# Optimization experiments

Hardware: AMD Instinct MI355X
Metric: run time of the kernel (lower is better)

## Reference

```python
import jax, jax.numpy as jnp
import numpy as np

N_NODES = 50000
N_EDGES = 800000
IN_CH, HID_CH, OUT_CH = 128, 256, 128


def _glorot(key, shape):
    fan_in, fan_out = shape[1], shape[0]
    lim = float(np.sqrt(6.0 / (fan_in + fan_out)))
    return jax.random.uniform(key, shape, jnp.float32, -lim, lim)


def setup_inputs() -> dict:
    key = jax.random.key(0)
    ks = jax.random.split(key, 8)
    x = jax.random.normal(ks[0], (N_NODES, IN_CH), jnp.float32)
    edge_index = jax.random.randint(ks[1], (2, N_EDGES), 0, N_NODES, jnp.int64)
    return {
        "x": x,
        "edge_index": edge_index,
        # layer 1: SAGEConv(128 -> 256): lin_l (with bias) on aggregated, lin_r (no bias) on root
        "W1l": _glorot(ks[2], (HID_CH, IN_CH)),
        "b1l": jnp.zeros((HID_CH,), jnp.float32),
        "W1r": _glorot(ks[3], (HID_CH, IN_CH)),
        # layer 2: SAGEConv(256 -> 128)
        "W2l": _glorot(ks[4], (OUT_CH, HID_CH)),
        "b2l": jnp.zeros((OUT_CH,), jnp.float32),
        "W2r": _glorot(ks[5], (OUT_CH, HID_CH)),
    }


def _sage_conv(x, src, dst, Wl, bl, Wr, n_nodes):
    # mean-aggregate neighbor (source) features at destination nodes
    msg = x[src]                                                   # [E, C] gather
    agg = jax.ops.segment_sum(msg, dst, num_segments=n_nodes)      # [N, C]
    deg = jax.ops.segment_sum(jnp.ones((src.shape[0],), x.dtype), dst,
                              num_segments=n_nodes)                # [N]
    mean = agg / jnp.maximum(deg, 1.0)[:, None]                    # zero-degree -> 0
    return mean @ Wl.T + bl + x @ Wr.T


def reference(x, edge_index, W1l, b1l, W1r, W2l, b2l, W2r):
    src, dst = edge_index[0], edge_index[1]
    n = x.shape[0]
    h = _sage_conv(x, src, dst, W1l, b1l, W1r, n)
    h = jax.nn.relu(h)  # dropout is identity in eval mode
    out = _sage_conv(h, src, dst, W2l, b2l, W2r, n)
    return out
```

## Files before the change

kernel.cpp:

```cpp
#include <hip/hip_runtime.h>

#define N_NODES 50000
#define IN_CH   128
#define HID_CH  256
#define OUT_CH  128

#define NB    196
#define NWG   64
#define NBNW  (NB * NWG)
#define SCHUNK 49

#define XBLK  3125
#define WBLK  64

typedef __attribute__((ext_vector_type(8))) short bf16x8;
typedef __attribute__((ext_vector_type(4))) float f32x4;
typedef __attribute__((ext_vector_type(2))) float f32x2;

__device__ __forceinline__ unsigned short f32_bf16_rne(float f) {
    unsigned u = __float_as_uint(f);
    unsigned r = u + 0x7fff + ((u >> 16) & 1);
    return (unsigned short)(r >> 16);
}

__device__ __forceinline__ void cvt8(const float* __restrict__ in,
                                     unsigned short* __restrict__ outp, size_t j)
{
    const float4* p = reinterpret_cast<const float4*>(in) + 2 * j;
    float4 a = p[0], b = p[1];
    alignas(16) unsigned short t[8] = {
        f32_bf16_rne(a.x), f32_bf16_rne(a.y), f32_bf16_rne(a.z), f32_bf16_rne(a.w),
        f32_bf16_rne(b.x), f32_bf16_rne(b.y), f32_bf16_rne(b.z), f32_bf16_rne(b.w)};
    *reinterpret_cast<int4*>(outp + 8 * j) = *reinterpret_cast<const int4*>(t);
}

__global__ __launch_bounds__(256) void prep_kernel(
    const int* __restrict__ src, const int* __restrict__ dst,
    int* __restrict__ counts, int E, int chunk,
    const float* __restrict__ x, unsigned short* __restrict__ xb,
    unsigned char* __restrict__ xb8,
    const float* __restrict__ W1l, const float* __restrict__ W1r,
    const float* __restrict__ W2l, const float* __restrict__ W2r,
    unsigned short* __restrict__ W1lb, unsigned short* __restrict__ W1rb,
    unsigned short* __restrict__ W2lb, unsigned short* __restrict__ W2rb)
{
    const int b = blockIdx.x;
    if (b < NWG) {
        __shared__ int h[NB];
        for (int i = threadIdx.x; i < NB; i += 256) h[i] = 0;
        __syncthreads();
        const int e0 = b * chunk;
        const int e1 = min(e0 + chunk, E);
        for (int e = e0 + threadIdx.x; e < e1; e += 256) {
            int s = src[e], d = dst[e];
            if ((unsigned)s < (unsigned)N_NODES && (unsigned)d < (unsigned)N_NODES)
                atomicAdd(&h[d >> 8], 1);
        }
        __syncthreads();
        for (int i = threadIdx.x; i < NB; i += 256)
            counts[i * NWG + b] = h[i];
    } else if (b < NWG + XBLK) {
        size_t j = (size_t)(b - NWG) * 256 + threadIdx.x;
        const float4* p = reinterpret_cast<const float4*>(x) + 2 * j;
        float4 a = p[0], bb = p[1];
        alignas(16) unsigned short t[8] = {
            f32_bf16_rne(a.x),  f32_bf16_rne(a.y),  f32_bf16_rne(a.z),  f32_bf16_rne(a.w),
            f32_bf16_rne(bb.x), f32_bf16_rne(bb.y), f32_bf16_rne(bb.z), f32_bf16_rne(bb.w)};
        *reinterpret_cast<int4*>(xb + 8 * j) = *reinterpret_cast<const int4*>(t);
        unsigned u0 = __builtin_amdgcn_cvt_pk_fp8_f32(a.x, a.y, 0, false);
        u0 = __builtin_amdgcn_cvt_pk_fp8_f32(a.z, a.w, u0, true);
        unsigned u1 = __builtin_amdgcn_cvt_pk_fp8_f32(bb.x, bb.y, 0, false);
        u1 = __builtin_amdgcn_cvt_pk_fp8_f32(bb.z, bb.w, u1, true);
        uint2 uv; uv.x = u0; uv.y = u1;
        *reinterpret_cast<uint2*>(xb8 + 8 * j) = uv;
    } else {
        int idx = (b - NWG - XBLK) * 256 + threadIdx.x;
        int seg = idx >> 12, j = idx & 4095;
        const float* in = (seg == 0) ? W1l : (seg == 1) ? W1r : (seg == 2) ? W2l : W2r;
        unsigned short* o = (seg == 0) ? W1lb : (seg == 1) ? W1rb : (seg == 2) ? W2lb : W2rb;
        cvt8(in, o, (size_t)j);
    }
}

__global__ __launch_bounds__(256) void scan_all_kernel(
    const int* __restrict__ counts, int* __restrict__ S)
{
    __shared__ int tot[256];
    const int t = threadIdx.x;
    const int base = t * SCHUNK;
    int loc[SCHUNK];
    int sum = 0;
#pragma unroll
    for (int k = 0; k < SCHUNK; ++k) {
        loc[k] = sum;
        sum += counts[base + k];
    }
    tot[t] = sum;
    __syncthreads();
    for (int off = 1; off < 256; off <<= 1) {
        int v = (t >= off) ? tot[t - off] : 0;
        __syncthreads();
        if (t >= off) tot[t] += v;
        __syncthreads();
    }
    int offv = (t == 0) ? 0 : tot[t - 1];
#pragma unroll
    for (int k = 0; k < SCHUNK; ++k)
        S[base + k] = loc[k] + offv;
    if (t == 255) S[NBNW] = offv + sum;
}

__global__ __launch_bounds__(256) void bscatter_kernel(
    const int* __restrict__ src, const int* __restrict__ dst,
    const int* __restrict__ S, int* __restrict__ pairs, int E, int chunk)
{
    __shared__ int cur[NB];
    const int w = blockIdx.x;
    for (int i = threadIdx.x; i < NB; i += 256) cur[i] = S[i * NWG + w];
    __syncthreads();
    const int e0 = w * chunk;
    const int e1 = min(e0 + chunk, E);
    for (int e = e0 + threadIdx.x; e < e1; e += 256) {
        int s = src[e], d = dst[e];
        if ((unsigned)s < (unsigned)N_NODES && (unsigned)d < (unsigned)N_NODES) {
            int pos = atomicAdd(&cur[d >> 8], 1);
            pairs[pos] = (s << 8) | (d & 255);
        }
    }
}

__global__ __launch_bounds__(256) void bsort_kernel(
    const int* __restrict__ pairs, const int* __restrict__ S,
    int* __restrict__ rowptr, int* __restrict__ colidx)
{
    __shared__ int hcnt[256];
    __shared__ int hcur[256];
    const int b = blockIdx.x;
    const int start = S[b * NWG];
    const int endv  = (b == NB - 1) ? S[NBNW] : S[(b + 1) * NWG];

    hcnt[threadIdx.x] = 0;
    __syncthreads();
    for (int e = start + threadIdx.x; e < endv; e += 256)
        atomicAdd(&hcnt[pairs[e] & 255], 1);
    __syncthreads();
    for (int off = 1; off < 256; off <<= 1) {
        int t = (threadIdx.x >= off) ? hcnt[threadIdx.x - off] : 0;
        __syncthreads();
        if (threadIdx.x >= off) hcnt[threadIdx.x] += t;
        __syncthreads();
    }
    int offv = (threadIdx.x == 0) ? 0 : hcnt[threadIdx.x - 1];
    hcur[threadIdx.x] = offv;
    int node = (b << 8) + threadIdx.x;
    if (node < N_NODES) rowptr[node] = start + offv;
    if (b == NB - 1 && threadIdx.x == 0) rowptr[N_NODES] = endv;
    __syncthreads();
    for (int e = start + threadIdx.x; e < endv; e += 256) {
        int p = pairs[e];
        int pos = atomicAdd(&hcur[p & 255], 1);
        colidx[start + pos] = (unsigned)p >> 8;
    }
}

#define ACC8(v)                                                              \
    { f32x2 t0 = __builtin_amdgcn_cvt_pk_f32_fp8(v.x, false);                \
      f32x2 t1 = __builtin_amdgcn_cvt_pk_f32_fp8(v.x, true);                 \
      f32x2 t2 = __builtin_amdgcn_cvt_pk_f32_fp8(v.y, false);                \
      f32x2 t3 = __builtin_amdgcn_cvt_pk_f32_fp8(v.y, true);                 \
      acc[0] += t0.x; acc[1] += t0.y; acc[2] += t1.x; acc[3] += t1.y;        \
      acc[4] += t2.x; acc[5] += t2.y; acc[6] += t3.x; acc[7] += t3.y; }

#define AGG_BODY(CH)                                                            \
    const int node = blockIdx.x * 4 + (threadIdx.x >> 6);                       \
    if (node >= N_NODES) return;                                                \
    const int lane = threadIdx.x & 63;                                          \
    const int grp = lane >> 4, ch = lane & 15;                                  \
    const int beg = rowptr[node], end = rowptr[node + 1];                       \
    const int len = end - beg;                                                  \
    const int q = (len + 3) >> 2;                                               \
    int j  = beg + grp * q;                                                     \
    int j1 = min(j + q, end);                                                   \
    float acc[8] = {};                                                          \
    for (; j + 3 < j1; j += 4) {                                                \
        int s0 = colidx[j],     s1 = colidx[j + 1];                             \
        int s2 = colidx[j + 2], s3 = colidx[j + 3];                             \
        uint2 v0 = *reinterpret_cast<const uint2*>(feat + (size_t)s0 * CH + ch * 8); \
        uint2 v1 = *reinterpret_cast<const uint2*>(feat + (size_t)s1 * CH + ch * 8); \
        uint2 v2 = *reinterpret_cast<const uint2*>(feat + (size_t)s2 * CH + ch * 8); \
        uint2 v3 = *reinterpret_cast<const uint2*>(feat + (size_t)s3 * CH + ch * 8); \
        ACC8(v0) ACC8(v1) ACC8(v2) ACC8(v3)                                     \
    }                                                                           \
    for (; j < j1; ++j) {                                                       \
        int s0 = colidx[j];                                                     \
        uint2 v0 = *reinterpret_cast<const uint2*>(feat + (size_t)s0 * CH + ch * 8); \
        ACC8(v0)                                                                \
    }                                                                           \
    _Pragma("unroll")                                                           \
    for (int k = 0; k < 8; ++k) {                                               \
        acc[k] += __shfl_xor(acc[k], 16);                                       \
        acc[k] += __shfl_xor(acc[k], 32);                                       \
    }                                                                           \
    const float sc = 1.0f / fmaxf((float)len, 1.0f);

__global__ __launch_bounds__(256) void agg1_kernel(
    const unsigned char* __restrict__ feat, const int* __restrict__ rowptr,
    const int* __restrict__ colidx, unsigned short* __restrict__ outp)
{
    AGG_BODY(IN_CH)
    if (grp == 0) {
        alignas(16) unsigned short t[8];
#pragma unroll
        for (int k = 0; k < 8; ++k) t[k] = f32_bf16_rne(acc[k] * sc);
        *reinterpret_cast<int4*>(outp + (size_t)node * IN_CH + ch * 8) =
            *reinterpret_cast<const int4*>(t);
    }
}

__global__ __launch_bounds__(256) void agg2_kernel(
    const unsigned char* __restrict__ feat, const int* __restrict__ rowptr,
    const int* __restrict__ colidx, float* __restrict__ out)
{
    AGG_BODY(OUT_CH)
    if (grp == 0) {
        float* o = out + (size_t)node * OUT_CH + ch * 8;
        float4 o0 = reinterpret_cast<float4*>(o)[0];
        float4 o1 = reinterpret_cast<float4*>(o)[1];
        o0.x += acc[0] * sc; o0.y += acc[1] * sc; o0.z += acc[2] * sc; o0.w += acc[3] * sc;
        o1.x += acc[4] * sc; o1.y += acc[5] * sc; o1.z += acc[6] * sc; o1.w += acc[7] * sc;
        reinterpret_cast<float4*>(o)[0] = o0;
        reinterpret_cast<float4*>(o)[1] = o1;
    }
}

__device__ __forceinline__ void stage_async(
    const unsigned short* __restrict__ g, int ldg, int rowBase, int maxRow,
    int kBase, unsigned short* __restrict__ s, int tid)
{
    const int wave = tid >> 6;
    const int lane = tid & 63;
    const int r_in = lane >> 3;
    const int c_g  = (lane & 7) ^ r_in;
#pragma unroll
    for (int it = 0; it < 4; ++it) {
        const int rowBlk = it * 32 + wave * 8;
        int row = rowBase + rowBlk + r_in;
        if (row >= maxRow) row = maxRow - 1;
        const unsigned short* gp = g + (size_t)row * ldg + kBase + c_g * 8;
        unsigned short* lp = s + rowBlk * 64;
        __builtin_amdgcn_global_load_lds(
            (const __attribute__((address_space(1))) unsigned int*)gp,
            (__attribute__((address_space(3))) unsigned int*)lp,
            16, 0, 0);
    }
}

__device__ __forceinline__ const bf16x8* frag_ptr(
    const unsigned short* __restrict__ s, int rr, int c)
{
    return reinterpret_cast<const bf16x8*>(s + rr * 64 + (((c ^ (rr & 7))) << 3));
}

__device__ __forceinline__ void mfma_tile(
    const unsigned short* __restrict__ As, const unsigned short* __restrict__ Bs,
    int wm, int wn, int l16, int quad, f32x4 acc[4][4])
{
#pragma unroll
    for (int k0 = 0; k0 < 64; k0 += 32) {
        const int c = (k0 >> 3) + quad;
        bf16x8 a[4], b[4];
#pragma unroll
        for (int i = 0; i < 4; ++i)
            a[i] = *frag_ptr(As, wm * 64 + i * 16 + l16, c);
#pragma unroll
        for (int j = 0; j < 4; ++j)
            b[j] = *frag_ptr(Bs, wn * 64 + j * 16 + l16, c);
#pragma unroll
        for (int i = 0; i < 4; ++i)
#pragma unroll
            for (int j = 0; j < 4; ++j)
                acc[i][j] = __builtin_amdgcn_mfma_f32_16x16x32_bf16(
                    b[j], a[i], acc[i][j], 0, 0, 0);
    }
}

__global__ __launch_bounds__(256) void gemm1_mfma(
    const unsigned short* __restrict__ mean1b, const unsigned short* __restrict__ xb,
    const unsigned short* __restrict__ W1lb,   const unsigned short* __restrict__ W1rb,
    const float* __restrict__ b1l, unsigned short* __restrict__ hb)
{
    __shared__ unsigned short As[128 * 64];
    __shared__ unsigned short Bs[128 * 64];
    const int tid = threadIdx.x;
    const int wid = tid >> 6, lane = tid & 63;
    const int wm = wid & 1, wn = wid >> 1;
    const int l16 = lane & 15, quad = lane >> 4;
    const int rowBase = blockIdx.x * 128;
    const int colBase = blockIdx.y * 128;

    f32x4 z = {0.f, 0.f, 0.f, 0.f};
    f32x4 acc[4][4];
#pragma unroll
    for (int i = 0; i < 4; ++i)
#pragma unroll
        for (int j = 0; j < 4; ++j) acc[i][j] = z;

#pragma unroll
    for (int op = 0; op < 2; ++op) {
        const unsigned short* A = op ? xb : mean1b;
        const unsigned short* B = op ? W1rb : W1lb;
#pragma unroll
        for (int kb = 0; kb < IN_CH; kb += 64) {
            __syncthreads();
            stage_async(A, IN_CH, rowBase, N_NODES, kb, As, tid);
            stage_async(B, IN_CH, colBase, HID_CH, kb, Bs, tid);
            __syncthreads();
            mfma_tile(As, Bs, wm, wn, l16, quad, acc);
        }
    }

#pragma unroll
    for (int i = 0; i < 4; ++i) {
        int m = rowBase + wm * 64 + i * 16 + l16;
        if (m >= N_NODES) continue;
#pragma unroll
        for (int j = 0; j < 4; ++j) {
            int col = colBase + wn * 64 + j * 16 + quad * 4;
            float4 bv = *reinterpret_cast<const float4*>(b1l + col);
            alignas(8) unsigned short t[4];
            t[0] = f32_bf16_rne(fmaxf(acc[i][j][0] + bv.x, 0.0f));
            t[1] = f32_bf16_rne(fmaxf(acc[i][j][1] + bv.y, 0.0f));
            t[2] = f32_bf16_rne(fmaxf(acc[i][j][2] + bv.z, 0.0f));
            t[3] = f32_bf16_rne(fmaxf(acc[i][j][3] + bv.w, 0.0f));
            *reinterpret_cast<uint2*>(hb + (size_t)m * HID_CH + col) =
                *reinterpret_cast<const uint2*>(t);
        }
    }
}

__global__ __launch_bounds__(256) void gemm2_mfma(
    const unsigned short* __restrict__ hb, const unsigned short* __restrict__ W2lb,
    const unsigned short* __restrict__ W2rb, const float* __restrict__ b2l,
    unsigned char* __restrict__ pb8, float* __restrict__ out)
{
    __shared__ unsigned short As[128 * 64];
    __shared__ unsigned short Bs[128 * 64];
    const int tid = threadIdx.x;
    const int wid = tid >> 6, lane = tid & 63;
    const int wm = wid & 1, wn = wid >> 1;
    const int l16 = lane & 15, quad = lane >> 4;
    const int rowBase = blockIdx.x * 128;
    const unsigned short* B = blockIdx.y ? W2rb : W2lb;

    f32x4 z = {0.f, 0.f, 0.f, 0.f};
    f32x4 acc[4][4];
#pragma unroll
    for (int i = 0; i < 4; ++i)
#pragma unroll
        for (int j = 0; j < 4; ++j) acc[i][j] = z;

#pragma unroll
    for (int kb = 0; kb < HID_CH; kb += 64) {
        __syncthreads();
        stage_async(hb, HID_CH, rowBase, N_NODES, kb, As, tid);
        stage_async(B, HID_CH, 0, OUT_CH, kb, Bs, tid);
        __syncthreads();
        mfma_tile(As, Bs, wm, wn, l16, quad, acc);
    }

    if (blockIdx.y == 0) {
#pragma unroll
        for (int i = 0; i < 4; ++i) {
            int m = rowBase + wm * 64 + i * 16 + l16;
            if (m >= N_NODES) continue;
#pragma unroll
            for (int j = 0; j < 4; ++j) {
                int col = wn * 64 + j * 16 + quad * 4;
                unsigned u = __builtin_amdgcn_cvt_pk_fp8_f32(
                    acc[i][j][0], acc[i][j][1], 0, false);
                u = __builtin_amdgcn_cvt_pk_fp8_f32(
                    acc[i][j][2], acc[i][j][3], u, true);
                *reinterpret_cast<unsigned*>(pb8 + (size_t)m * OUT_CH + col) = u;
            }
        }
    } else {
#pragma unroll
        for (int i = 0; i < 4; ++i) {
            int m = rowBase + wm * 64 + i * 16 + l16;
            if (m >= N_NODES) continue;
#pragma unroll
            for (int j = 0; j < 4; ++j) {
                int col = wn * 64 + j * 16 + quad * 4;
                float4 bv = *reinterpret_cast<const float4*>(b2l + col);
                float4 o;
                o.x = acc[i][j][0] + bv.x;
                o.y = acc[i][j][1] + bv.y;
                o.z = acc[i][j][2] + bv.z;
                o.w = acc[i][j][3] + bv.w;
                *reinterpret_cast<float4*>(out + (size_t)m * OUT_CH + col) = o;
            }
        }
    }
}

extern "C" void kernel_launch(void* const* d_in, const int* in_sizes, int n_in,
                              void* d_out, int out_size, void* d_ws, size_t ws_size,
                              hipStream_t stream)
{
    const float* x   = (const float*)d_in[0];
    const int*   ei  = (const int*)d_in[1];
    const float* W1l = (const float*)d_in[2];
    const float* b1l = (const float*)d_in[3];
    const float* W1r = (const float*)d_in[4];
    const float* W2l = (const float*)d_in[5];
    const float* b2l = (const float*)d_in[6];
    const float* W2r = (const float*)d_in[7];

    const int E = in_sizes[1] / 2;
    const int* src = ei;
    const int* dst = ei + E;

    char* ws = (char*)d_ws;
    size_t off = 0;
    auto alloc = [&](size_t bytes) {
        void* p = ws + off;
        off += (bytes + 255) & ~(size_t)255;
        return p;
    };
    unsigned short* xb     = (unsigned short*)alloc((size_t)N_NODES * IN_CH * 2);
    unsigned char*  xb8    = (unsigned char*)alloc((size_t)N_NODES * IN_CH);
    unsigned short* mean1b = (unsigned short*)alloc((size_t)N_NODES * IN_CH * 2);
    unsigned short* hb     = (unsigned short*)alloc((size_t)N_NODES * HID_CH * 2);
    unsigned char*  pb8    = (unsigned char*)alloc((size_t)N_NODES * OUT_CH);
    unsigned short* W1lb   = (unsigned short*)alloc((size_t)HID_CH * IN_CH * 2);
    unsigned short* W1rb   = (unsigned short*)alloc((size_t)HID_CH * IN_CH * 2);
    unsigned short* W2lb   = (unsigned short*)alloc((size_t)OUT_CH * HID_CH * 2);
    unsigned short* W2rb   = (unsigned short*)alloc((size_t)OUT_CH * HID_CH * 2);
    int* counts = (int*)alloc((size_t)NBNW * 4);
    int* S      = (int*)alloc((size_t)(NBNW + 1) * 4);
    int* pairs  = (int*)alloc((size_t)E * 4);
    int* rowptr = (int*)alloc((size_t)(N_NODES + 1) * 4);
    int* colidx = (int*)alloc((size_t)E * 4);
    float* out = (float*)d_out;

    const int chunk = (E + NWG - 1) / NWG;

    prep_kernel<<<NWG + XBLK + WBLK, 256, 0, stream>>>(
        src, dst, counts, E, chunk, x, xb, xb8,
        W1l, W1r, W2l, W2r, W1lb, W1rb, W2lb, W2rb);
    scan_all_kernel<<<1, 256, 0, stream>>>(counts, S);
    bscatter_kernel<<<NWG, 256, 0, stream>>>(src, dst, S, pairs, E, chunk);
    bsort_kernel<<<NB, 256, 0, stream>>>(pairs, S, rowptr, colidx);

    const int aggBlocks = (N_NODES + 3) / 4;
    const int mBlocks = (N_NODES + 127) / 128;

    agg1_kernel<<<aggBlocks, 256, 0, stream>>>(xb8, rowptr, colidx, mean1b);
    gemm1_mfma<<<dim3(mBlocks, HID_CH / 128), 256, 0, stream>>>(
        mean1b, xb, W1lb, W1rb, b1l, hb);
    gemm2_mfma<<<dim3(mBlocks, 2), 256, 0, stream>>>(hb, W2lb, W2rb, b2l, pb8, out);
    agg2_kernel<<<aggBlocks, 256, 0, stream>>>(pb8, rowptr, colidx, out);
}
```

Measured before the change: 235.1 us.

## Replace two-level bucket sort CSR build with atomic counting sort; 16 lanes per node aggregation

The CSR construction drops the bucketed histogram, scan, scatter and per-bucket sort. It now uses global per-node atomic degree counts, a single-block scan over all 50000 nodes, and an atomic scatter of source ids into colidx. The neighbour aggregation now assigns 16 lanes per node instead of 64 split into four groups, and broadcasts column indices with sub-wave shuffles, which removes the cross-group reductions. This cuts kernel launches and a pass over a pairs buffer, but brings heavy global atomic contention, a serial single-block scan over many elements, and a non-deterministic neighbour order.

Result: slower. 399.0 us (+69.7%).

```diff
diff --git a/kernel.cpp b/kernel.cpp
--- a/kernel.cpp
+++ b/kernel.cpp
@@ -5,13 +5,10 @@
 #define HID_CH  256
 #define OUT_CH  128
 
-#define NB    196
 #define NWG   64
-#define NBNW  (NB * NWG)
-#define SCHUNK 49
-
 #define XBLK  3125
 #define WBLK  64
+#define SCHUNK 196
 
 typedef __attribute__((ext_vector_type(8))) short bf16x8;
 typedef __attribute__((ext_vector_type(4))) float f32x4;
@@ -46,19 +43,13 @@
 {
     const int b = blockIdx.x;
     if (b < NWG) {
-        __shared__ int h[NB];
-        for (int i = threadIdx.x; i < NB; i += 256) h[i] = 0;
-        __syncthreads();
         const int e0 = b * chunk;
         const int e1 = min(e0 + chunk, E);
         for (int e = e0 + threadIdx.x; e < e1; e += 256) {
             int s = src[e], d = dst[e];
             if ((unsigned)s < (unsigned)N_NODES && (unsigned)d < (unsigned)N_NODES)
-                atomicAdd(&h[d >> 8], 1);
-        }
-        __syncthreads();
-        for (int i = threadIdx.x; i < NB; i += 256)
-            counts[i * NWG + b] = h[i];
+                atomicAdd(&counts[d], 1);
+        }
     } else if (b < NWG + XBLK) {
         size_t j = (size_t)(b - NWG) * 256 + threadIdx.x;
         const float4* p = reinterpret_cast<const float4*>(x) + 2 * j;
@@ -82,18 +73,16 @@
     }
 }
 
-__global__ __launch_bounds__(256) void scan_all_kernel(
-    const int* __restrict__ counts, int* __restrict__ S)
+__global__ __launch_bounds__(256) void scan_kernel(
+    const int* __restrict__ counts, int* __restrict__ rowptr, int* __restrict__ cur)
 {
     __shared__ int tot[256];
     const int t = threadIdx.x;
     const int base = t * SCHUNK;
-    int loc[SCHUNK];
     int sum = 0;
-#pragma unroll
     for (int k = 0; k < SCHUNK; ++k) {
-        loc[k] = sum;
-        sum += counts[base + k];
+        int i = base + k;
+        if (i < N_NODES) sum += counts[i];
     }
     tot[t] = sum;
     __syncthreads();
@@ -103,63 +92,30 @@
         if (t >= off) tot[t] += v;
         __syncthreads();
     }
-    int offv = (t == 0) ? 0 : tot[t - 1];
-#pragma unroll
-    for (int k = 0; k < SCHUNK; ++k)
-        S[base + k] = loc[k] + offv;
-    if (t == 255) S[NBNW] = offv + sum;
-}
-
-__global__ __launch_bounds__(256) void bscatter_kernel(
+    int run = (t == 0) ? 0 : tot[t - 1];
+    for (int k = 0; k < SCHUNK; ++k) {
+        int i = base + k;
+        if (i < N_NODES) {
+            rowptr[i] = run;
+            cur[i]    = run;
+            run += counts[i];
+        }
+    }
+    if (t == 255) rowptr[N_NODES] = run;
+}
+
+__global__ __launch_bounds__(256) void scatter_kernel(
     const int* __restrict__ src, const int* __restrict__ dst,
-    const int* __restrict__ S, int* __restrict__ pairs, int E, int chunk)
-{
-    __shared__ int cur[NB];
-    const int w = blockIdx.x;
-    for (int i = threadIdx.x; i < NB; i += 256) cur[i] = S[i * NWG + w];
-    __syncthreads();
-    const int e0 = w * chunk;
-    const int e1 = min(e0 + chunk, E);
-    for (int e = e0 + threadIdx.x; e < e1; e += 256) {
+    int* __restrict__ cur, int* __restrict__ colidx, int E)
+{
+    int i = blockIdx.x * 256 + threadIdx.x;
+    const int stride = gridDim.x * 256;
+    for (int e = i; e < E; e += stride) {
         int s = src[e], d = dst[e];
         if ((unsigned)s < (unsigned)N_NODES && (unsigned)d < (unsigned)N_NODES) {
-            int pos = atomicAdd(&cur[d >> 8], 1);
-            pairs[pos] = (s << 8) | (d & 255);
-        }
-    }
-}
-
-__global__ __launch_bounds__(256) void bsort_kernel(
-    const int* __restrict__ pairs, const int* __restrict__ S,
-    int* __restrict__ rowptr, int* __restrict__ colidx)
-{
-    __shared__ int hcnt[256];
-    __shared__ int hcur[256];
-    const int b = blockIdx.x;
-    const int start = S[b * NWG];
-    const int endv  = (b == NB - 1) ? S[NBNW] : S[(b + 1) * NWG];
-
-    hcnt[threadIdx.x] = 0;
-    __syncthreads();
-    for (int e = start + threadIdx.x; e < endv; e += 256)
-        atomicAdd(&hcnt[pairs[e] & 255], 1);
-    __syncthreads();
-    for (int off = 1; off < 256; off <<= 1) {
-        int t = (threadIdx.x >= off) ? hcnt[threadIdx.x - off] : 0;
-        __syncthreads();
-        if (threadIdx.x >= off) hcnt[threadIdx.x] += t;
-        __syncthreads();
-    }
-    int offv = (threadIdx.x == 0) ? 0 : hcnt[threadIdx.x - 1];
-    hcur[threadIdx.x] = offv;
-    int node = (b << 8) + threadIdx.x;
-    if (node < N_NODES) rowptr[node] = start + offv;
-    if (b == NB - 1 && threadIdx.x == 0) rowptr[N_NODES] = endv;
-    __syncthreads();
-    for (int e = start + threadIdx.x; e < endv; e += 256) {
-        int p = pairs[e];
-        int pos = atomicAdd(&hcur[p & 255], 1);
-        colidx[start + pos] = (unsigned)p >> 8;
+            int pos = atomicAdd(&cur[d], 1);
+            colidx[pos] = s;
+        }
     }
 }
 
@@ -172,34 +128,30 @@
       acc[4] += t2.x; acc[5] += t2.y; acc[6] += t3.x; acc[7] += t3.y; }
 
 #define AGG_BODY(CH)                                                            \
-    const int node = blockIdx.x * 4 + (threadIdx.x >> 6);                       \
+    const int node = blockIdx.x * 16 + (threadIdx.x >> 4);                      \
     if (node >= N_NODES) return;                                                \
-    const int lane = threadIdx.x & 63;                                          \
-    const int grp = lane >> 4, ch = lane & 15;                                  \
+    const int l8 = threadIdx.x & 15;                                            \
     const int beg = rowptr[node], end = rowptr[node + 1];                       \
     const int len = end - beg;                                                  \
-    const int q = (len + 3) >> 2;                                               \
-    int j  = beg + grp * q;                                                     \
-    int j1 = min(j + q, end);                                                   \
     float acc[8] = {};                                                          \
-    for (; j + 3 < j1; j += 4) {                                                \
-        int s0 = colidx[j],     s1 = colidx[j + 1];                             \
-        int s2 = colidx[j + 2], s3 = colidx[j + 3];                             \
-        uint2 v0 = *reinterpret_cast<const uint2*>(feat + (size_t)s0 * CH + ch * 8); \
-        uint2 v1 = *reinterpret_cast<const uint2*>(feat + (size_t)s1 * CH + ch * 8); \
-        uint2 v2 = *reinterpret_cast<const uint2*>(feat + (size_t)s2 * CH + ch * 8); \
-        uint2 v3 = *reinterpret_cast<const uint2*>(feat + (size_t)s3 * CH + ch * 8); \
-        ACC8(v0) ACC8(v1) ACC8(v2) ACC8(v3)                                     \
-    }                                                                           \
-    for (; j < j1; ++j) {                                                       \
-        int s0 = colidx[j];                                                     \
-        uint2 v0 = *reinterpret_cast<const uint2*>(feat + (size_t)s0 * CH + ch * 8); \
-        ACC8(v0)                                                                \
-    }                                                                           \
-    _Pragma("unroll")                                                           \
-    for (int k = 0; k < 8; ++k) {                                               \
-        acc[k] += __shfl_xor(acc[k], 16);                                       \
-        acc[k] += __shfl_xor(acc[k], 32);                                       \
+    for (int base = beg; base < end; base += 16) {                              \
+        const int cnt = min(16, end - base);                                    \
+        int ci = colidx[base + ((l8 < cnt) ? l8 : 0)];                          \
+        int k = 0;                                                              \
+        for (; k + 3 < cnt; k += 4) {                                           \
+            int s0 = __shfl(ci, k, 16),     s1 = __shfl(ci, k + 1, 16);         \
+            int s2 = __shfl(ci, k + 2, 16), s3 = __shfl(ci, k + 3, 16);         \
+            uint2 v0 = *reinterpret_cast<const uint2*>(feat + (size_t)s0 * CH + l8 * 8); \
+            uint2 v1 = *reinterpret_cast<const uint2*>(feat + (size_t)s1 * CH + l8 * 8); \
+            uint2 v2 = *reinterpret_cast<const uint2*>(feat + (size_t)s2 * CH + l8 * 8); \
+            uint2 v3 = *reinterpret_cast<const uint2*>(feat + (size_t)s3 * CH + l8 * 8); \
+            ACC8(v0) ACC8(v1) ACC8(v2) ACC8(v3)                                 \
+        }                                                                       \
+        for (; k < cnt; ++k) {                                                  \
+            int s0 = __shfl(ci, k, 16);                                         \
+            uint2 v0 = *reinterpret_cast<const uint2*>(feat + (size_t)s0 * CH + l8 * 8); \
+            ACC8(v0)                                                            \
+        }                                                                       \
     }                                                                           \
     const float sc = 1.0f / fmaxf((float)len, 1.0f);
 
@@ -208,13 +160,11 @@
     const int* __restrict__ colidx, unsigned short* __restrict__ outp)
 {
     AGG_BODY(IN_CH)
-    if (grp == 0) {
-        alignas(16) unsigned short t[8];
-#pragma unroll
-        for (int k = 0; k < 8; ++k) t[k] = f32_bf16_rne(acc[k] * sc);
-        *reinterpret_cast<int4*>(outp + (size_t)node * IN_CH + ch * 8) =
-            *reinterpret_cast<const int4*>(t);
-    }
+    alignas(16) unsigned short t[8];
+#pragma unroll
+    for (int k = 0; k < 8; ++k) t[k] = f32_bf16_rne(acc[k] * sc);
+    *reinterpret_cast<int4*>(outp + (size_t)node * IN_CH + l8 * 8) =
+        *reinterpret_cast<const int4*>(t);
 }
 
 __global__ __launch_bounds__(256) void agg2_kernel(
@@ -222,15 +172,13 @@
     const int* __restrict__ colidx, float* __restrict__ out)
 {
     AGG_BODY(OUT_CH)
-    if (grp == 0) {
-        float* o = out + (size_t)node * OUT_CH + ch * 8;
-        float4 o0 = reinterpret_cast<float4*>(o)[0];
-        float4 o1 = reinterpret_cast<float4*>(o)[1];
-        o0.x += acc[0] * sc; o0.y += acc[1] * sc; o0.z += acc[2] * sc; o0.w += acc[3] * sc;
-        o1.x += acc[4] * sc; o1.y += acc[5] * sc; o1.z += acc[6] * sc; o1.w += acc[7] * sc;
-        reinterpret_cast<float4*>(o)[0] = o0;
-        reinterpret_cast<float4*>(o)[1] = o1;
-    }
+    float* o = out + (size_t)node * OUT_CH + l8 * 8;
+    float4 o0 = reinterpret_cast<float4*>(o)[0];
+    float4 o1 = reinterpret_cast<float4*>(o)[1];
+    o0.x += acc[0] * sc; o0.y += acc[1] * sc; o0.z += acc[2] * sc; o0.w += acc[3] * sc;
+    o1.x += acc[4] * sc; o1.y += acc[5] * sc; o1.z += acc[6] * sc; o1.w += acc[7] * sc;
+    reinterpret_cast<float4*>(o)[0] = o0;
+    reinterpret_cast<float4*>(o)[1] = o1;
 }
 
 __device__ __forceinline__ void stage_async(
@@ -436,23 +384,22 @@
     unsigned short* W1rb   = (unsigned short*)alloc((size_t)HID_CH * IN_CH * 2);
     unsigned short* W2lb   = (unsigned short*)alloc((size_t)OUT_CH * HID_CH * 2);
     unsigned short* W2rb   = (unsigned short*)alloc((size_t)OUT_CH * HID_CH * 2);
-    int* counts = (int*)alloc((size_t)NBNW * 4);
-    int* S      = (int*)alloc((size_t)(NBNW + 1) * 4);
-    int* pairs  = (int*)alloc((size_t)E * 4);
+    int* counts = (int*)alloc((size_t)N_NODES * 4);
     int* rowptr = (int*)alloc((size_t)(N_NODES + 1) * 4);
+    int* cur    = (int*)alloc((size_t)N_NODES * 4);
     int* colidx = (int*)alloc((size_t)E * 4);
     float* out = (float*)d_out;
 
     const int chunk = (E + NWG - 1) / NWG;
 
+    hipMemsetAsync(counts, 0, (size_t)N_NODES * 4, stream);
     prep_kernel<<<NWG + XBLK + WBLK, 256, 0, stream>>>(
         src, dst, counts, E, chunk, x, xb, xb8,
         W1l, W1r, W2l, W2r, W1lb, W1rb, W2lb, W2rb);
-    scan_all_kernel<<<1, 256, 0, stream>>>(counts, S);
-    bscatter_kernel<<<NWG, 256, 0, stream>>>(src, dst, S, pairs, E, chunk);
-    bsort_kernel<<<NB, 256, 0, stream>>>(pairs, S, rowptr, colidx);
-
-    const int aggBlocks = (N_NODES + 3) / 4;
+    scan_kernel<<<1, 256, 0, stream>>>(counts, rowptr, cur);
+    scatter_kernel<<<2048, 256, 0, stream>>>(src, dst, cur, colidx, E);
+
+    const int aggBlocks = (N_NODES + 15) / 16;
     const int mBlocks = (N_NODES + 127) / 128;
 
     agg1_kernel<<<aggBlocks, 256, 0, stream>>>(xb8, rowptr, colidx, mean1b);
```

## Map one 16-lane group per node in aggregation, broadcast neighbor indices via shuffles

Applied to the files above, without the earlier changes.

The aggregation kernels now assign 16 lanes per destination node, 16 nodes per block, instead of a 64-lane wave split into four edge partitions per node. This removes the cross-group shuffle reduction and the idle lanes during output. Each group loads up to 16 column indices cooperatively and broadcasts them with width-16 shuffles, replacing redundant per-lane index loads. In exchange, each node's edges are processed serially by one group, so per-node memory parallelism drops while more nodes run concurrently.

Result: faster. 219.6 us (-6.6%).

```diff
diff --git a/kernel.cpp b/kernel.cpp
--- a/kernel.cpp
+++ b/kernel.cpp
@@ -172,34 +172,30 @@
       acc[4] += t2.x; acc[5] += t2.y; acc[6] += t3.x; acc[7] += t3.y; }
 
 #define AGG_BODY(CH)                                                            \
-    const int node = blockIdx.x * 4 + (threadIdx.x >> 6);                       \
+    const int node = blockIdx.x * 16 + (threadIdx.x >> 4);                      \
     if (node >= N_NODES) return;                                                \
-    const int lane = threadIdx.x & 63;                                          \
-    const int grp = lane >> 4, ch = lane & 15;                                  \
+    const int l8 = threadIdx.x & 15;                                            \
     const int beg = rowptr[node], end = rowptr[node + 1];                       \
     const int len = end - beg;                                                  \
-    const int q = (len + 3) >> 2;                                               \
-    int j  = beg + grp * q;                                                     \
-    int j1 = min(j + q, end);                                                   \
     float acc[8] = {};                                                          \
-    for (; j + 3 < j1; j += 4) {                                                \
-        int s0 = colidx[j],     s1 = colidx[j + 1];                             \
-        int s2 = colidx[j + 2], s3 = colidx[j + 3];                             \
-        uint2 v0 = *reinterpret_cast<const uint2*>(feat + (size_t)s0 * CH + ch * 8); \
-        uint2 v1 = *reinterpret_cast<const uint2*>(feat + (size_t)s1 * CH + ch * 8); \
-        uint2 v2 = *reinterpret_cast<const uint2*>(feat + (size_t)s2 * CH + ch * 8); \
-        uint2 v3 = *reinterpret_cast<const uint2*>(feat + (size_t)s3 * CH + ch * 8); \
-        ACC8(v0) ACC8(v1) ACC8(v2) ACC8(v3)                                     \
-    }                                                                           \
-    for (; j < j1; ++j) {                                                       \
-        int s0 = colidx[j];                                                     \
-        uint2 v0 = *reinterpret_cast<const uint2*>(feat + (size_t)s0 * CH + ch * 8); \
-        ACC8(v0)                                                                \
-    }                                                                           \
-    _Pragma("unroll")                                                           \
-    for (int k = 0; k < 8; ++k) {                                               \
-        acc[k] += __shfl_xor(acc[k], 16);                                       \
-        acc[k] += __shfl_xor(acc[k], 32);                                       \
+    for (int base = beg; base < end; base += 16) {                              \
+        const int cnt = min(16, end - base);                                    \
+        int ci = colidx[base + ((l8 < cnt) ? l8 : 0)];                          \
+        int k = 0;                                                              \
+        for (; k + 3 < cnt; k += 4) {                                           \
+            int s0 = __shfl(ci, k, 16),     s1 = __shfl(ci, k + 1, 16);         \
+            int s2 = __shfl(ci, k + 2, 16), s3 = __shfl(ci, k + 3, 16);         \
+            uint2 v0 = *reinterpret_cast<const uint2*>(feat + (size_t)s0 * CH + l8 * 8); \
+            uint2 v1 = *reinterpret_cast<const uint2*>(feat + (size_t)s1 * CH + l8 * 8); \
+            uint2 v2 = *reinterpret_cast<const uint2*>(feat + (size_t)s2 * CH + l8 * 8); \
+            uint2 v3 = *reinterpret_cast<const uint2*>(feat + (size_t)s3 * CH + l8 * 8); \
+            ACC8(v0) ACC8(v1) ACC8(v2) ACC8(v3)                                 \
+        }                                                                       \
+        for (; k < cnt; ++k) {                                                  \
+            int s0 = __shfl(ci, k, 16);                                         \
+            uint2 v0 = *reinterpret_cast<const uint2*>(feat + (size_t)s0 * CH + l8 * 8); \
+            ACC8(v0)                                                            \
+        }                                                                       \
     }                                                                           \
     const float sc = 1.0f / fmaxf((float)len, 1.0f);
 
@@ -208,13 +204,11 @@
     const int* __restrict__ colidx, unsigned short* __restrict__ outp)
 {
     AGG_BODY(IN_CH)
-    if (grp == 0) {
-        alignas(16) unsigned short t[8];
-#pragma unroll
-        for (int k = 0; k < 8; ++k) t[k] = f32_bf16_rne(acc[k] * sc);
-        *reinterpret_cast<int4*>(outp + (size_t)node * IN_CH + ch * 8) =
-            *reinterpret_cast<const int4*>(t);
-    }
+    alignas(16) unsigned short t[8];
+#pragma unroll
+    for (int k = 0; k < 8; ++k) t[k] = f32_bf16_rne(acc[k] * sc);
+    *reinterpret_cast<int4*>(outp + (size_t)node * IN_CH + l8 * 8) =
+        *reinterpret_cast<const int4*>(t);
 }
 
 __global__ __launch_bounds__(256) void agg2_kernel(
@@ -222,15 +216,13 @@
     const int* __restrict__ colidx, float* __restrict__ out)
 {
     AGG_BODY(OUT_CH)
-    if (grp == 0) {
-        float* o = out + (size_t)node * OUT_CH + ch * 8;
-        float4 o0 = reinterpret_cast<float4*>(o)[0];
-        float4 o1 = reinterpret_cast<float4*>(o)[1];
-        o0.x += acc[0] * sc; o0.y += acc[1] * sc; o0.z += acc[2] * sc; o0.w += acc[3] * sc;
-        o1.x += acc[4] * sc; o1.y += acc[5] * sc; o1.z += acc[6] * sc; o1.w += acc[7] * sc;
-        reinterpret_cast<float4*>(o)[0] = o0;
-        reinterpret_cast<float4*>(o)[1] = o1;
-    }
+    float* o = out + (size_t)node * OUT_CH + l8 * 8;
+    float4 o0 = reinterpret_cast<float4*>(o)[0];
+    float4 o1 = reinterpret_cast<float4*>(o)[1];
+    o0.x += acc[0] * sc; o0.y += acc[1] * sc; o0.z += acc[2] * sc; o0.w += acc[3] * sc;
+    o1.x += acc[4] * sc; o1.y += acc[5] * sc; o1.z += acc[6] * sc; o1.w += acc[7] * sc;
+    reinterpret_cast<float4*>(o)[0] = o0;
+    reinterpret_cast<float4*>(o)[1] = o1;
 }
 
 __device__ __forceinline__ void stage_async(
@@ -452,7 +444,7 @@
     bscatter_kernel<<<NWG, 256, 0, stream>>>(src, dst, S, pairs, E, chunk);
     bsort_kernel<<<NB, 256, 0, stream>>>(pairs, S, rowptr, colidx);
 
-    const int aggBlocks = (N_NODES + 3) / 4;
+    const int aggBlocks = (N_NODES + 15) / 16;
     const int mBlocks = (N_NODES + 127) / 128;
 
     agg1_kernel<<<aggBlocks, 256, 0, stream>>>(xb8, rowptr, colidx, mean1b);
```
